# Kernel tuning notes

Hardware: AMD Instinct MI355X
Metric: run time of the kernel (lower is better)

The kernel has to match this reference:

```python
import jax, jax.numpy as jnp
import numpy as np

Q = 8192      # num query tokens
S = 32768     # num support points
E = 131072    # num edges (query<-support neighbor pairs)
D = 256       # token_dim
H = 8         # num_heads
HD = D // H   # head_dim = 32
GEO = 128     # geo mlp_hidden = geo_dim
FFN = 2 * D   # ffn hidden
STAT_IN = 12  # 4 stats * 3 coords
EPS_LN = 1e-5


def gelu(x):
    return jax.nn.gelu(x, approximate=False)  # torch nn.GELU default (erf)


def layernorm(x, g, b):
    m = jnp.mean(x, axis=-1, keepdims=True)
    v = jnp.mean((x - m) ** 2, axis=-1, keepdims=True)
    return (x - m) * jax.lax.rsqrt(v + EPS_LN) * g + b


def setup_inputs() -> dict:
    key = jax.random.key(0)
    ks = jax.random.split(key, 16)
    w = lambda k, shp: jax.random.normal(k, shp, jnp.float32) * 0.02
    return {
        "query_tokens": jax.random.normal(ks[0], (Q, D), jnp.float32),
        "query_pos": jax.random.normal(ks[1], (Q, 3), jnp.float32),
        "support_feats": jax.random.normal(ks[2], (S, D), jnp.float32),
        "support_pos": jax.random.normal(ks[3], (S, 3), jnp.float32),
        "Wq": w(ks[4], (D, D)), "Wk": w(ks[5], (D, D)), "Wv": w(ks[6], (D, D)),
        "Wg": w(ks[7], (GEO, D)),
        "Wo": w(ks[8], (D, D)), "bo": jnp.zeros((D,), jnp.float32),
        "log_tau": jnp.array(0.0, jnp.float32),
        "ln1_g": jnp.ones((D,), jnp.float32), "ln1_b": jnp.zeros((D,), jnp.float32),
        "ln2_g": jnp.ones((D,), jnp.float32), "ln2_b": jnp.zeros((D,), jnp.float32),
        "Wf1": w(ks[9], (D, FFN)), "bf1": jnp.zeros((FFN,), jnp.float32),
        "Wf2": w(ks[10], (FFN, D)), "bf2": jnp.zeros((D,), jnp.float32),
        "Gw1": w(ks[11], (STAT_IN, GEO)), "Gb1": jnp.zeros((GEO,), jnp.float32),
        "Gw2": w(ks[12], (GEO, GEO)), "Gb2": jnp.zeros((GEO,), jnp.float32),
        "q_idx": jnp.sort(jax.random.randint(ks[13], (E,), 0, Q)),
        "s_idx": jax.random.randint(ks[14], (E,), 0, S),
        "num_queries": Q,
    }


def geo_stats(rel, q_idx, num_q):
    # rel: [E,3] relative positions; segmented mean/std/min/max -> [num_q, 12]
    ones = jnp.ones((rel.shape[0], 1), rel.dtype)
    cnt = jnp.maximum(jax.ops.segment_sum(ones, q_idx, num_q), 1.0)  # [Q,1]
    mean = jax.ops.segment_sum(rel, q_idx, num_q) / cnt
    var = jax.ops.segment_sum((rel - mean[q_idx]) ** 2, q_idx, num_q) / cnt
    std = jnp.sqrt(var)
    # torch inits min/max with +/-inf then clamps to [-100,100]; jax segment
    # min/max init with dtype extremes -> same result after clip
    mn = jnp.clip(jax.ops.segment_min(rel, q_idx, num_q), -100.0, 100.0)
    mx = jnp.clip(jax.ops.segment_max(rel, q_idx, num_q), -100.0, 100.0)
    return jnp.concatenate([mean, std, mn, mx], axis=-1)


def reference(query_tokens, query_pos, support_feats, support_pos,
              Wq, Wk, Wv, Wg, Wo, bo, log_tau,
              ln1_g, ln1_b, ln2_g, ln2_b,
              Wf1, bf1, Wf2, bf2, Gw1, Gb1, Gw2, Gb2,
              q_idx, s_idx, num_queries):
    num_q = num_queries
    # ---- statistical geo embedding ----
    rel = support_pos[s_idx] - query_pos[q_idx]                 # [E,3]
    raw = geo_stats(rel, q_idx, num_q)                          # [Q,12]
    geo = gelu(gelu(raw @ Gw1 + Gb1) @ Gw2 + Gb2)               # [Q,GEO]

    # ---- AGNO cross attention (pre-norm) ----
    qt = layernorm(query_tokens, ln1_g, ln1_b)
    Qf = qt @ Wq                                                # [Q,D]
    Kf = support_feats @ Wk                                     # [S,D]
    Vf = support_feats @ Wv                                     # [S,D]
    Gf = geo @ Wg                                               # [Q,D]
    qh = Qf[q_idx].reshape(E, H, HD)
    kh = Kf[s_idx].reshape(E, H, HD)
    vh = Vf[s_idx].reshape(E, H, HD)
    gh = Gf[q_idx].reshape(E, H, HD)
    tau = jnp.exp(log_tau)
    scores = jnp.sum(qh * kh, axis=-1) / (jnp.sqrt(jnp.float32(HD)) * tau)  # [E,H]
    # torch scores_max starts at 0 -> max(0, segment max)
    smax = jnp.maximum(jax.ops.segment_max(scores, q_idx, num_q), 0.0)
    ex = jnp.exp(scores - smax[q_idx])
    ssum = jax.ops.segment_sum(ex, q_idx, num_q)
    alpha = ex / jnp.maximum(ssum[q_idx], 1e-8)                 # [E,H]
    weighted = alpha[..., None] * (vh + gh)                     # [E,H,HD]
    out = jax.ops.segment_sum(weighted, q_idx, num_q)           # [Q,H,HD]
    attn = out.reshape(num_q, D) @ Wo + bo

    # ---- residual + FFN ----
    x = query_tokens + attn
    x = x + gelu(layernorm(x, ln2_g, ln2_b) @ Wf1 + bf1) @ Wf2 + bf2
    return x
```

## Files before the change

### kernel.cpp

```cpp
#include <hip/hip_runtime.h>
#include <math.h>

#define QN 8192
#define SN 32768
#define EN 131072
#define DN 256
#define HN 8
#define HDN 32
#define GEON 128
#define FFNN 512

typedef __attribute__((ext_vector_type(8))) short bf16x8;
typedef __attribute__((ext_vector_type(8))) unsigned short u16x8;
typedef __attribute__((ext_vector_type(4))) unsigned short u16x4;
typedef __attribute__((ext_vector_type(4))) float f32x4;

__device__ __forceinline__ unsigned short f2b(float f) {
  union { float f; unsigned u; } v; v.f = f;
  unsigned u = v.u;
  u += 0x7fffu + ((u >> 16) & 1u);
  return (unsigned short)(u >> 16);
}
__device__ __forceinline__ float b2f(unsigned short h) {
  union { unsigned u; float f; } v; v.u = ((unsigned)h) << 16; return v.f;
}
__device__ __forceinline__ float gelu_f(float x) {
  return 0.5f * x * (1.0f + erff(x * 0.70710678118654752440f));
}

template <int KT>
__device__ __forceinline__ u16x8* lds_gk(unsigned short* base, int row, int col) {
  int g = (col >> 3) ^ (row & 7);
  return reinterpret_cast<u16x8*>(base + row * KT + g * 8);
}

__global__ __launch_bounds__(256) void transpose_weights(
    const float* Wq, const float* Wk, const float* Wv, const float* Wg,
    const float* Wo, const float* Wf1, const float* Wf2,
    unsigned short* WqT, unsigned short* WkvT, unsigned short* WgT,
    unsigned short* WoT, unsigned short* Wf1T, unsigned short* Wf2T) {
  int b = blockIdx.x;
  const float* src; unsigned short* dst; int K, N, tile;
  if (b < 16)       { src = Wq;  dst = WqT;          K = 256; N = 256; tile = b; }
  else if (b < 32)  { src = Wk;  dst = WkvT;         K = 256; N = 256; tile = b - 16; }
  else if (b < 48)  { src = Wv;  dst = WkvT + 65536; K = 256; N = 256; tile = b - 32; }
  else if (b < 56)  { src = Wg;  dst = WgT;          K = 128; N = 256; tile = b - 48; }
  else if (b < 72)  { src = Wo;  dst = WoT;          K = 256; N = 256; tile = b - 56; }
  else if (b < 104) { src = Wf1; dst = Wf1T;         K = 256; N = 512; tile = b - 72; }
  else              { src = Wf2; dst = Wf2T;         K = 512; N = 256; tile = b - 104; }
  int ktiles = K >> 6;
  int k0 = (tile % ktiles) * 64, n0 = (tile / ktiles) * 64;
  __shared__ float ts[64][65];
  int t = threadIdx.x;
  int c4 = (t & 15) * 4;
  int r = t >> 4;
#pragma unroll
  for (int p = 0; p < 4; ++p) {
    int row = p * 16 + r;
    float4 v = *(const float4*)(src + (size_t)(k0 + row) * N + n0 + c4);
    ts[row][c4 + 0] = v.x; ts[row][c4 + 1] = v.y;
    ts[row][c4 + 2] = v.z; ts[row][c4 + 3] = v.w;
  }
  __syncthreads();
#pragma unroll
  for (int p = 0; p < 4; ++p) {
    int n = p * 16 + r;
    ushort4 o;
    o.x = f2b(ts[c4 + 0][n]); o.y = f2b(ts[c4 + 1][n]);
    o.z = f2b(ts[c4 + 2][n]); o.w = f2b(ts[c4 + 3][n]);
    *(ushort4*)(dst + (size_t)(n0 + n) * K + k0 + c4) = o;
  }
}

__global__ __launch_bounds__(256) void seg_offsets(const int* q_idx, int* offs) {
  int i = blockIdx.x * 256 + threadIdx.x;
  if (i > QN) return;
  int lo = 0, hi = EN;
  while (lo < hi) {
    int mid = (lo + hi) >> 1;
    if (q_idx[mid] < i) lo = mid + 1; else hi = mid;
  }
  offs[i] = lo;
}

__global__ __launch_bounds__(256) void geo_stats_kernel(
    const float* qpos, const float* spos, const int* offs, const int* s_idx, float* raw) {
  int q = blockIdx.x * 64 + (threadIdx.x >> 2);
  int sub = threadIdx.x & 3;
  int e0 = offs[q], e1 = offs[q + 1];
  float qx = qpos[q * 3 + 0], qy = qpos[q * 3 + 1], qz = qpos[q * 3 + 2];
  float cnt = 0.f, sx = 0.f, sy = 0.f, sz = 0.f, sxx = 0.f, syy = 0.f, szz = 0.f;
  float mnx = 1e30f, mny = 1e30f, mnz = 1e30f, mxx = -1e30f, mxy = -1e30f, mxz = -1e30f;
  for (int e = e0 + sub; e < e1; e += 4) {
    int s = s_idx[e];
    float rx = spos[s * 3 + 0] - qx;
    float ry = spos[s * 3 + 1] - qy;
    float rz = spos[s * 3 + 2] - qz;
    cnt += 1.f;
    sx += rx; sy += ry; sz += rz;
    sxx += rx * rx; syy += ry * ry; szz += rz * rz;
    mnx = fminf(mnx, rx); mny = fminf(mny, ry); mnz = fminf(mnz, rz);
    mxx = fmaxf(mxx, rx); mxy = fmaxf(mxy, ry); mxz = fmaxf(mxz, rz);
  }
#pragma unroll
  for (int msk = 1; msk <= 2; msk <<= 1) {
    cnt += __shfl_xor(cnt, msk);
    sx += __shfl_xor(sx, msk); sy += __shfl_xor(sy, msk); sz += __shfl_xor(sz, msk);
    sxx += __shfl_xor(sxx, msk); syy += __shfl_xor(syy, msk); szz += __shfl_xor(szz, msk);
    mnx = fminf(mnx, __shfl_xor(mnx, msk));
    mny = fminf(mny, __shfl_xor(mny, msk));
    mnz = fminf(mnz, __shfl_xor(mnz, msk));
    mxx = fmaxf(mxx, __shfl_xor(mxx, msk));
    mxy = fmaxf(mxy, __shfl_xor(mxy, msk));
    mxz = fmaxf(mxz, __shfl_xor(mxz, msk));
  }
  if (sub == 0) {
    float c = fmaxf(cnt, 1.f);
    float mx_ = sx / c, my_ = sy / c, mz_ = sz / c;
    float vx = fmaxf(sxx / c - mx_ * mx_, 0.f);
    float vy = fmaxf(syy / c - my_ * my_, 0.f);
    float vz = fmaxf(szz / c - mz_ * mz_, 0.f);
    float* r = raw + (size_t)q * 12;
    r[0] = mx_; r[1] = my_; r[2] = mz_;
    r[3] = sqrtf(vx); r[4] = sqrtf(vy); r[5] = sqrtf(vz);
    r[6] = fminf(fmaxf(mnx, -100.f), 100.f);
    r[7] = fminf(fmaxf(mny, -100.f), 100.f);
    r[8] = fminf(fmaxf(mnz, -100.f), 100.f);
    r[9] = fminf(fmaxf(mxx, -100.f), 100.f);
    r[10] = fminf(fmaxf(mxy, -100.f), 100.f);
    r[11] = fminf(fmaxf(mxz, -100.f), 100.f);
  }
}

__global__ __launch_bounds__(128) void geo_mlp_kernel(
    const float* raw, const float* Gw1, const float* Gb1,
    const float* Gw2, const float* Gb2, unsigned short* geo_b) {
  int qb = blockIdx.x * 8;
  int j = threadIdx.x;
  __shared__ float rs[8][12];
  __shared__ float h1[8][128];
  if (j < 96) rs[j / 12][j % 12] = raw[(size_t)(qb + j / 12) * 12 + (j % 12)];
  __syncthreads();
  float b1 = Gb1[j];
  float acc[8];
#pragma unroll
  for (int qq = 0; qq < 8; ++qq) acc[qq] = b1;
  for (int i = 0; i < 12; ++i) {
    float w = Gw1[i * GEON + j];
#pragma unroll
    for (int qq = 0; qq < 8; ++qq) acc[qq] += rs[qq][i] * w;
  }
#pragma unroll
  for (int qq = 0; qq < 8; ++qq) h1[qq][j] = gelu_f(acc[qq]);
  __syncthreads();
  float b2 = Gb2[j];
  float acc2[8];
#pragma unroll
  for (int qq = 0; qq < 8; ++qq) acc2[qq] = b2;
  for (int k = 0; k < 128; ++k) {
    float w = Gw2[k * GEON + j];
#pragma unroll
    for (int qq = 0; qq < 8; ++qq) acc2[qq] += h1[qq][k] * w;
  }
#pragma unroll
  for (int qq = 0; qq < 8; ++qq)
    geo_b[(size_t)(qb + qq) * GEON + j] = f2b(gelu_f(acc2[qq]));
}

__global__ __launch_bounds__(256) void ln_kernel(
    const float* x, const float* g, const float* b, unsigned short* out) {
  int row = blockIdx.x * 4 + (threadIdx.x >> 6);
  int lane = threadIdx.x & 63;
  const float* xr = x + (size_t)row * DN;
  float4 v = *(const float4*)(xr + lane * 4);
  float s = v.x + v.y + v.z + v.w;
  float ss = v.x * v.x + v.y * v.y + v.z * v.z + v.w * v.w;
#pragma unroll
  for (int msk = 1; msk <= 32; msk <<= 1) {
    s += __shfl_xor(s, msk);
    ss += __shfl_xor(ss, msk);
  }
  float mean = s * (1.f / 256.f);
  float var = ss * (1.f / 256.f) - mean * mean;
  float rs = 1.0f / sqrtf(var + 1e-5f);
  float4 gg = *(const float4*)(g + lane * 4);
  float4 bb = *(const float4*)(b + lane * 4);
  unsigned short* o = out + (size_t)row * DN + lane * 4;
  o[0] = f2b((v.x - mean) * rs * gg.x + bb.x);
  o[1] = f2b((v.y - mean) * rs * gg.y + bb.y);
  o[2] = f2b((v.z - mean) * rs * gg.z + bb.z);
  o[3] = f2b((v.w - mean) * rs * gg.w + bb.w);
}

__global__ __launch_bounds__(256) void kv_gemm(
    const float* A, const unsigned short* BT, unsigned short* KVb) {
  __shared__ unsigned short As[64 * 256];
  __shared__ unsigned short Bs[32 * 256];
  int t = threadIdx.x;
  int bm = blockIdx.x * 64;
  int w = t >> 6, lane = t & 63;
  int quad = lane >> 4, l16 = lane & 15;
  int wr = w >> 1, wc = w & 1;
  int srow = t >> 2, sub = t & 3;
  {
    const float* Ag = A + (size_t)(bm + srow) * 256 + sub * 64;
#pragma unroll
    for (int i = 0; i < 8; ++i) {
      float4 f0 = *(const float4*)(Ag + i * 8);
      float4 f1 = *(const float4*)(Ag + i * 8 + 4);
      u16x8 u;
      u[0] = f2b(f0.x); u[1] = f2b(f0.y); u[2] = f2b(f0.z); u[3] = f2b(f0.w);
      u[4] = f2b(f1.x); u[5] = f2b(f1.y); u[6] = f2b(f1.z); u[7] = f2b(f1.w);
      *lds_gk<256>(As, srow, sub * 64 + i * 8) = u;
    }
  }
  int brow = t >> 3, bsub = t & 7;
  u16x8 pre[4];
  {
    const unsigned short* Bg = BT + (size_t)brow * 256 + bsub * 32;
#pragma unroll
    for (int i = 0; i < 4; ++i) pre[i] = *reinterpret_cast<const u16x8*>(Bg + i * 8);
  }
  for (int ct = 0; ct < 16; ++ct) {
#pragma unroll
    for (int i = 0; i < 4; ++i)
      *lds_gk<256>(Bs, brow, bsub * 32 + i * 8) = pre[i];
    __syncthreads();
    if (ct < 15) {
      const unsigned short* Bg = BT + (size_t)((ct + 1) * 32 + brow) * 256 + bsub * 32;
#pragma unroll
      for (int i = 0; i < 4; ++i) pre[i] = *reinterpret_cast<const u16x8*>(Bg + i * 8);
    }
    f32x4 acc[2];
    acc[0] = (f32x4){0.f, 0.f, 0.f, 0.f};
    acc[1] = (f32x4){0.f, 0.f, 0.f, 0.f};
#pragma unroll
    for (int k = 0; k < 8; ++k) {
      bf16x8 a0 = *reinterpret_cast<bf16x8*>(lds_gk<256>(As, wr * 32 + l16, k * 32 + quad * 8));
      bf16x8 a1 = *reinterpret_cast<bf16x8*>(lds_gk<256>(As, wr * 32 + 16 + l16, k * 32 + quad * 8));
      bf16x8 b0 = *reinterpret_cast<bf16x8*>(lds_gk<256>(Bs, wc * 16 + l16, k * 32 + quad * 8));
      acc[0] = __builtin_amdgcn_mfma_f32_16x16x32_bf16(a0, b0, acc[0], 0, 0, 0);
      acc[1] = __builtin_amdgcn_mfma_f32_16x16x32_bf16(a1, b0, acc[1], 0, 0, 0);
    }
#pragma unroll
    for (int i = 0; i < 2; ++i)
#pragma unroll
      for (int r = 0; r < 4; ++r) {
        int rw = bm + wr * 32 + i * 16 + quad * 4 + r;
        int col = ct * 32 + wc * 16 + l16;
        KVb[(size_t)rw * 512 + col] = f2b(acc[i][r]);
      }
    __syncthreads();
  }
}

template <bool A_FP32, bool COLGRID, bool HAS_BIAS, bool DO_GELU, bool HAS_RESID, bool STORE_F32>
__global__ __launch_bounds__(256) void gemm64(
    const void* Ap, const unsigned short* BT, int M, int N, int K,
    const float* bias, const float* resid, float* outF, unsigned short* outB) {
  __shared__ unsigned short As[64][40];
  __shared__ unsigned short Bs[64][40];
  int t = threadIdx.x;
  int bm = (COLGRID ? blockIdx.x : blockIdx.y) * 64;
  int bn = (COLGRID ? blockIdx.y : blockIdx.x) * 64;
  int w = t >> 6, lane = t & 63;
  int wr = w >> 1, wc = w & 1;
  int quad = lane >> 4, l16 = lane & 15;
  int row = t >> 2, chunk = t & 3;

  const float* AgF = (const float*)Ap + (size_t)(bm + row) * K + chunk * 8;
  const unsigned short* AgB = (const unsigned short*)Ap + (size_t)(bm + row) * K + chunk * 8;
  const unsigned short* Bg = BT + (size_t)(bn + row) * K + chunk * 8;

  float4 pf0, pf1;
  u16x8 pa, pb;
  if (A_FP32) { pf0 = *(const float4*)AgF; pf1 = *(const float4*)(AgF + 4); }
  else        { pa = *(const u16x8*)AgB; }
  pb = *(const u16x8*)Bg;

  f32x4 acc[2][2];
#pragma unroll
  for (int i = 0; i < 2; ++i)
#pragma unroll
    for (int j = 0; j < 2; ++j) acc[i][j] = (f32x4){0.f, 0.f, 0.f, 0.f};

  for (int k0 = 0; k0 < K; k0 += 32) {
    u16x8 ua;
    if (A_FP32) {
      ua[0] = f2b(pf0.x); ua[1] = f2b(pf0.y); ua[2] = f2b(pf0.z); ua[3] = f2b(pf0.w);
      ua[4] = f2b(pf1.x); ua[5] = f2b(pf1.y); ua[6] = f2b(pf1.z); ua[7] = f2b(pf1.w);
    } else {
      ua = pa;
    }
    *reinterpret_cast<u16x8*>(&As[row][chunk * 8]) = ua;
    *reinterpret_cast<u16x8*>(&Bs[row][chunk * 8]) = pb;
    __syncthreads();
    if (k0 + 32 < K) {
      if (A_FP32) { pf0 = *(const float4*)(AgF + k0 + 32); pf1 = *(const float4*)(AgF + k0 + 36); }
      else        { pa = *(const u16x8*)(AgB + k0 + 32); }
      pb = *(const u16x8*)(Bg + k0 + 32);
    }
    bf16x8 a0 = *reinterpret_cast<const bf16x8*>(&As[wr * 32 + l16][quad * 8]);
    bf16x8 a1 = *reinterpret_cast<const bf16x8*>(&As[wr * 32 + 16 + l16][quad * 8]);
    bf16x8 b0 = *reinterpret_cast<const bf16x8*>(&Bs[wc * 32 + l16][quad * 8]);
    bf16x8 b1 = *reinterpret_cast<const bf16x8*>(&Bs[wc * 32 + 16 + l16][quad * 8]);
    acc[0][0] = __builtin_amdgcn_mfma_f32_16x16x32_bf16(a0, b0, acc[0][0], 0, 0, 0);
    acc[0][1] = __builtin_amdgcn_mfma_f32_16x16x32_bf16(a0, b1, acc[0][1], 0, 0, 0);
    acc[1][0] = __builtin_amdgcn_mfma_f32_16x16x32_bf16(a1, b0, acc[1][0], 0, 0, 0);
    acc[1][1] = __builtin_amdgcn_mfma_f32_16x16x32_bf16(a1, b1, acc[1][1], 0, 0, 0);
    __syncthreads();
  }

#pragma unroll
  for (int i = 0; i < 2; ++i)
#pragma unroll
    for (int j = 0; j < 2; ++j) {
      int col = bn + wc * 32 + j * 16 + l16;
      float bv = HAS_BIAS ? bias[col] : 0.f;
#pragma unroll
      for (int r = 0; r < 4; ++r) {
        int rw = bm + wr * 32 + i * 16 + quad * 4 + r;
        float v = acc[i][j][r] + bv;
        if (DO_GELU) v = gelu_f(v);
        if (HAS_RESID) v += resid[(size_t)rw * N + col];
        if (STORE_F32) outF[(size_t)rw * N + col] = v;
        else outB[(size_t)rw * N + col] = f2b(v);
      }
    }
}

__global__ __launch_bounds__(256) void attn_edge_kernel(
    const unsigned short* Qb, const unsigned short* Gfb, const unsigned short* KVb,
    const int* s_idx, const int* offs, const float* log_tau, unsigned short* attn_b) {
  int q = blockIdx.x * 4 + (threadIdx.x >> 6);
  int lane = threadIdx.x & 63;
  int slot = lane >> 4;
  int sl = lane & 15;
  int d0 = sl * 16;
  int e0 = offs[q], e1 = offs[q + 1];
  float invs = expf(-log_tau[0]) * 0.17677669529663687f;
  u16x8 qu0 = *(const u16x8*)(Qb + (size_t)q * DN + d0);
  u16x8 qu1 = *(const u16x8*)(Qb + (size_t)q * DN + d0 + 8);
  u16x8 gu0 = *(const u16x8*)(Gfb + (size_t)q * DN + d0);
  u16x8 gu1 = *(const u16x8*)(Gfb + (size_t)q * DN + d0 + 8);
  float qf[16], gf[16];
#pragma unroll
  for (int j = 0; j < 8; ++j) {
    qf[j] = b2f(qu0[j]) * invs; qf[j + 8] = b2f(qu1[j]) * invs;
    gf[j] = b2f(gu0[j]);        gf[j + 8] = b2f(gu1[j]);
  }
  const float NEG = -1e30f;
  float m = -INFINITY, l = 0.f;
  float a[16];
#pragma unroll
  for (int j = 0; j < 16; ++j) a[j] = 0.f;
  for (int e = e0; e < e1; e += 4) {
    int ee = e + slot;
    bool valid = ee < e1;
    int s = s_idx[valid ? ee : (e1 - 1)];
    const unsigned short* kr = KVb + (size_t)s * 512 + d0;
    u16x8 ku0 = *(const u16x8*)kr;
    u16x8 ku1 = *(const u16x8*)(kr + 8);
    u16x8 vu0 = *(const u16x8*)(kr + 256);
    u16x8 vu1 = *(const u16x8*)(kr + 264);
    float p = 0.f;
#pragma unroll
    for (int j = 0; j < 8; ++j) {
      p += qf[j] * b2f(ku0[j]);
      p += qf[j + 8] * b2f(ku1[j]);
    }
    p += __shfl_xor(p, 1);
    if (!valid) p = -INFINITY;
    float mnew = fmaxf(m, p);
    float sc = (m > NEG) ? __expf(m - mnew) : 0.f;
    float we = valid ? __expf(p - mnew) : 0.f;
    l = l * sc + we;
#pragma unroll
    for (int j = 0; j < 8; ++j) {
      a[j] = a[j] * sc + we * b2f(vu0[j]);
      a[j + 8] = a[j + 8] * sc + we * b2f(vu1[j]);
    }
    m = mnew;
  }
#pragma unroll
  for (int msk = 16; msk <= 32; msk <<= 1) {
    float om = __shfl_xor(m, msk);
    float ol = __shfl_xor(l, msk);
    float M2 = fmaxf(m, om);
    float ws = (m > NEG) ? __expf(m - M2) : 0.f;
    float wo = (om > NEG) ? __expf(om - M2) : 0.f;
    l = l * ws + ol * wo;
#pragma unroll
    for (int j = 0; j < 16; ++j) {
      float oa = __shfl_xor(a[j], msk);
      a[j] = a[j] * ws + oa * wo;
    }
    m = M2;
  }
  float M = fmaxf(m, 0.f);
  float em = (m > NEG) ? __expf(m - M) : 0.f;
  float denom = fmaxf(l * em, 1e-8f);
  float f = em / denom;
  float sa = l * f;
  if (slot == 0) {
    u16x8 o0, o1;
#pragma unroll
    for (int j = 0; j < 8; ++j) {
      o0[j] = f2b(a[j] * f + gf[j] * sa);
      o1[j] = f2b(a[j + 8] * f + gf[j + 8] * sa);
    }
    *(u16x8*)(attn_b + (size_t)q * DN + d0) = o0;
    *(u16x8*)(attn_b + (size_t)q * DN + d0 + 8) = o1;
  }
}

extern "C" void kernel_launch(void* const* d_in, const int* in_sizes, int n_in,
                              void* d_out, int out_size, void* d_ws, size_t ws_size,
                              hipStream_t stream) {
  const float* query_tokens  = (const float*)d_in[0];
  const float* query_pos     = (const float*)d_in[1];
  const float* support_feats = (const float*)d_in[2];
  const float* support_pos   = (const float*)d_in[3];
  const float* Wq  = (const float*)d_in[4];
  const float* Wk  = (const float*)d_in[5];
  const float* Wv  = (const float*)d_in[6];
  const float* Wg  = (const float*)d_in[7];
  const float* Wo  = (const float*)d_in[8];
  const float* bo  = (const float*)d_in[9];
  const float* log_tau = (const float*)d_in[10];
  const float* ln1_g = (const float*)d_in[11];
  const float* ln1_b = (const float*)d_in[12];
  const float* ln2_g = (const float*)d_in[13];
  const float* ln2_b = (const float*)d_in[14];
  const float* Wf1 = (const float*)d_in[15];
  const float* bf1 = (const float*)d_in[16];
  const float* Wf2 = (const float*)d_in[17];
  const float* bf2 = (const float*)d_in[18];
  const float* Gw1 = (const float*)d_in[19];
  const float* Gb1 = (const float*)d_in[20];
  const float* Gw2 = (const float*)d_in[21];
  const float* Gb2 = (const float*)d_in[22];
  const int* q_idx = (const int*)d_in[23];
  const int* s_idx = (const int*)d_in[24];
  float* out = (float*)d_out;

  char* ws = (char*)d_ws;
  size_t off = 0;
  auto alloc = [&](size_t bytes) -> void* {
    void* p = ws + off;
    off = (off + bytes + 255) & ~(size_t)255;
    return p;
  };
  unsigned short* WqT  = (unsigned short*)alloc(65536 * 2);
  unsigned short* WkvT = (unsigned short*)alloc(131072 * 2);
  unsigned short* WgT  = (unsigned short*)alloc(32768 * 2);
  unsigned short* WoT  = (unsigned short*)alloc(65536 * 2);
  unsigned short* Wf1T = (unsigned short*)alloc(131072 * 2);
  unsigned short* Wf2T = (unsigned short*)alloc(131072 * 2);
  int* offs            = (int*)alloc((QN + 1) * 4);
  float* raw           = (float*)alloc((size_t)QN * 12 * 4);
  unsigned short* geo_b = (unsigned short*)alloc((size_t)QN * GEON * 2);
  unsigned short* qt_b  = (unsigned short*)alloc((size_t)QN * DN * 2);
  unsigned short* Qb    = (unsigned short*)alloc((size_t)QN * DN * 2);
  unsigned short* Gf_b  = (unsigned short*)alloc((size_t)QN * DN * 2);
  unsigned short* KVb   = (unsigned short*)alloc((size_t)SN * 512 * 2);
  unsigned short* attn_b = (unsigned short*)alloc((size_t)QN * DN * 2);
  float* x1             = (float*)alloc((size_t)QN * DN * 4);
  unsigned short* z_b   = (unsigned short*)alloc((size_t)QN * DN * 2);
  unsigned short* h_b   = (unsigned short*)alloc((size_t)QN * FFNN * 2);

  transpose_weights<<<136, 256, 0, stream>>>(Wq, Wk, Wv, Wg, Wo, Wf1, Wf2,
                                             WqT, WkvT, WgT, WoT, Wf1T, Wf2T);
  seg_offsets<<<33, 256, 0, stream>>>(q_idx, offs);
  geo_stats_kernel<<<QN / 64, 256, 0, stream>>>(query_pos, support_pos, offs, s_idx, raw);
  geo_mlp_kernel<<<QN / 8, 128, 0, stream>>>(raw, Gw1, Gb1, Gw2, Gb2, geo_b);
  ln_kernel<<<QN / 4, 256, 0, stream>>>(query_tokens, ln1_g, ln1_b, qt_b);
  kv_gemm<<<SN / 64, 256, 0, stream>>>(support_feats, WkvT, KVb);
  gemm64<false, true, false, false, false, false><<<dim3(QN / 64, DN / 64), 256, 0, stream>>>(
      qt_b, WqT, QN, DN, 256, nullptr, nullptr, nullptr, Qb);
  gemm64<false, true, false, false, false, false><<<dim3(QN / 64, DN / 64), 256, 0, stream>>>(
      geo_b, WgT, QN, DN, 128, nullptr, nullptr, nullptr, Gf_b);
  attn_edge_kernel<<<QN / 4, 256, 0, stream>>>(Qb, Gf_b, KVb, s_idx, offs, log_tau, attn_b);
  gemm64<false, true, true, false, true, true><<<dim3(QN / 64, DN / 64), 256, 0, stream>>>(
      attn_b, WoT, QN, DN, 256, bo, query_tokens, x1, nullptr);
  ln_kernel<<<QN / 4, 256, 0, stream>>>(x1, ln2_g, ln2_b, z_b);
  gemm64<false, true, true, true, false, false><<<dim3(QN / 64, FFNN / 64), 256, 0, stream>>>(
      z_b, Wf1T, QN, FFNN, 256, bf1, nullptr, nullptr, h_b);
  gemm64<false, true, true, false, true, true><<<dim3(QN / 64, DN / 64), 256, 0, stream>>>(
      h_b, Wf2T, QN, DN, 512, bf2, x1, out, nullptr);

  (void)in_sizes; (void)n_in; (void)out_size; (void)ws_size;
}
```

Measured before the change: 247.8 us.

## Merge prep and projection kernels into two heterogeneous fused launches

Folds the weight transpose, segment-offset search and first layernorm into one launch that picks its role from the block index. A second launch does the geo stats, geo MLP and the Wg projection in one block per 64 queries, with the geo features kept in swizzled LDS, and runs the KV and Q GEMMs alongside it. This removes several launches and the raw/geo_b global round trips. The cost is a larger shared-memory footprint (about 52KB) on every block of the second launch, which can lower occupancy for the KV/Q GEMM blocks, and 32-wide register accumulators in the geo MLP.

```diff
diff --git a/kernel.cpp b/kernel.cpp
--- a/kernel.cpp
+++ b/kernel.cpp
@@ -12,7 +12,6 @@
 
 typedef __attribute__((ext_vector_type(8))) short bf16x8;
 typedef __attribute__((ext_vector_type(8))) unsigned short u16x8;
-typedef __attribute__((ext_vector_type(4))) unsigned short u16x4;
 typedef __attribute__((ext_vector_type(4))) float f32x4;
 
 __device__ __forceinline__ unsigned short f2b(float f) {
@@ -33,138 +32,82 @@
   int g = (col >> 3) ^ (row & 7);
   return reinterpret_cast<u16x8*>(base + row * KT + g * 8);
 }
-
-__global__ __launch_bounds__(256) void transpose_weights(
+__device__ __forceinline__ unsigned short* lds_gs128(unsigned short* base, int row, int col) {
+  int g = (col >> 3) ^ (row & 7);
+  return base + row * 128 + g * 8 + (col & 7);
+}
+
+__global__ __launch_bounds__(256) void fused_prep(
     const float* Wq, const float* Wk, const float* Wv, const float* Wg,
     const float* Wo, const float* Wf1, const float* Wf2,
     unsigned short* WqT, unsigned short* WkvT, unsigned short* WgT,
-    unsigned short* WoT, unsigned short* Wf1T, unsigned short* Wf2T) {
+    unsigned short* WoT, unsigned short* Wf1T, unsigned short* Wf2T,
+    const int* q_idx, int* offs,
+    const float* x_ln, const float* lng, const float* lnb, unsigned short* ln_out) {
+  __shared__ float ts[64][65];
   int b = blockIdx.x;
-  const float* src; unsigned short* dst; int K, N, tile;
-  if (b < 16)       { src = Wq;  dst = WqT;          K = 256; N = 256; tile = b; }
-  else if (b < 32)  { src = Wk;  dst = WkvT;         K = 256; N = 256; tile = b - 16; }
-  else if (b < 48)  { src = Wv;  dst = WkvT + 65536; K = 256; N = 256; tile = b - 32; }
-  else if (b < 56)  { src = Wg;  dst = WgT;          K = 128; N = 256; tile = b - 48; }
-  else if (b < 72)  { src = Wo;  dst = WoT;          K = 256; N = 256; tile = b - 56; }
-  else if (b < 104) { src = Wf1; dst = Wf1T;         K = 256; N = 512; tile = b - 72; }
-  else              { src = Wf2; dst = Wf2T;         K = 512; N = 256; tile = b - 104; }
-  int ktiles = K >> 6;
-  int k0 = (tile % ktiles) * 64, n0 = (tile / ktiles) * 64;
-  __shared__ float ts[64][65];
   int t = threadIdx.x;
-  int c4 = (t & 15) * 4;
-  int r = t >> 4;
-#pragma unroll
-  for (int p = 0; p < 4; ++p) {
-    int row = p * 16 + r;
-    float4 v = *(const float4*)(src + (size_t)(k0 + row) * N + n0 + c4);
-    ts[row][c4 + 0] = v.x; ts[row][c4 + 1] = v.y;
-    ts[row][c4 + 2] = v.z; ts[row][c4 + 3] = v.w;
-  }
-  __syncthreads();
-#pragma unroll
-  for (int p = 0; p < 4; ++p) {
-    int n = p * 16 + r;
-    ushort4 o;
-    o.x = f2b(ts[c4 + 0][n]); o.y = f2b(ts[c4 + 1][n]);
-    o.z = f2b(ts[c4 + 2][n]); o.w = f2b(ts[c4 + 3][n]);
-    *(ushort4*)(dst + (size_t)(n0 + n) * K + k0 + c4) = o;
-  }
-}
-
-__global__ __launch_bounds__(256) void seg_offsets(const int* q_idx, int* offs) {
-  int i = blockIdx.x * 256 + threadIdx.x;
-  if (i > QN) return;
-  int lo = 0, hi = EN;
-  while (lo < hi) {
-    int mid = (lo + hi) >> 1;
-    if (q_idx[mid] < i) lo = mid + 1; else hi = mid;
-  }
-  offs[i] = lo;
-}
-
-__global__ __launch_bounds__(256) void geo_stats_kernel(
-    const float* qpos, const float* spos, const int* offs, const int* s_idx, float* raw) {
-  int q = blockIdx.x * 64 + (threadIdx.x >> 2);
-  int sub = threadIdx.x & 3;
-  int e0 = offs[q], e1 = offs[q + 1];
-  float qx = qpos[q * 3 + 0], qy = qpos[q * 3 + 1], qz = qpos[q * 3 + 2];
-  float cnt = 0.f, sx = 0.f, sy = 0.f, sz = 0.f, sxx = 0.f, syy = 0.f, szz = 0.f;
-  float mnx = 1e30f, mny = 1e30f, mnz = 1e30f, mxx = -1e30f, mxy = -1e30f, mxz = -1e30f;
-  for (int e = e0 + sub; e < e1; e += 4) {
-    int s = s_idx[e];
-    float rx = spos[s * 3 + 0] - qx;
-    float ry = spos[s * 3 + 1] - qy;
-    float rz = spos[s * 3 + 2] - qz;
-    cnt += 1.f;
-    sx += rx; sy += ry; sz += rz;
-    sxx += rx * rx; syy += ry * ry; szz += rz * rz;
-    mnx = fminf(mnx, rx); mny = fminf(mny, ry); mnz = fminf(mnz, rz);
-    mxx = fmaxf(mxx, rx); mxy = fmaxf(mxy, ry); mxz = fmaxf(mxz, rz);
-  }
-#pragma unroll
-  for (int msk = 1; msk <= 2; msk <<= 1) {
-    cnt += __shfl_xor(cnt, msk);
-    sx += __shfl_xor(sx, msk); sy += __shfl_xor(sy, msk); sz += __shfl_xor(sz, msk);
-    sxx += __shfl_xor(sxx, msk); syy += __shfl_xor(syy, msk); szz += __shfl_xor(szz, msk);
-    mnx = fminf(mnx, __shfl_xor(mnx, msk));
-    mny = fminf(mny, __shfl_xor(mny, msk));
-    mnz = fminf(mnz, __shfl_xor(mnz, msk));
-    mxx = fmaxf(mxx, __shfl_xor(mxx, msk));
-    mxy = fmaxf(mxy, __shfl_xor(mxy, msk));
-    mxz = fmaxf(mxz, __shfl_xor(mxz, msk));
-  }
-  if (sub == 0) {
-    float c = fmaxf(cnt, 1.f);
-    float mx_ = sx / c, my_ = sy / c, mz_ = sz / c;
-    float vx = fmaxf(sxx / c - mx_ * mx_, 0.f);
-    float vy = fmaxf(syy / c - my_ * my_, 0.f);
-    float vz = fmaxf(szz / c - mz_ * mz_, 0.f);
-    float* r = raw + (size_t)q * 12;
-    r[0] = mx_; r[1] = my_; r[2] = mz_;
-    r[3] = sqrtf(vx); r[4] = sqrtf(vy); r[5] = sqrtf(vz);
-    r[6] = fminf(fmaxf(mnx, -100.f), 100.f);
-    r[7] = fminf(fmaxf(mny, -100.f), 100.f);
-    r[8] = fminf(fmaxf(mnz, -100.f), 100.f);
-    r[9] = fminf(fmaxf(mxx, -100.f), 100.f);
-    r[10] = fminf(fmaxf(mxy, -100.f), 100.f);
-    r[11] = fminf(fmaxf(mxz, -100.f), 100.f);
-  }
-}
-
-__global__ __launch_bounds__(128) void geo_mlp_kernel(
-    const float* raw, const float* Gw1, const float* Gb1,
-    const float* Gw2, const float* Gb2, unsigned short* geo_b) {
-  int qb = blockIdx.x * 8;
-  int j = threadIdx.x;
-  __shared__ float rs[8][12];
-  __shared__ float h1[8][128];
-  if (j < 96) rs[j / 12][j % 12] = raw[(size_t)(qb + j / 12) * 12 + (j % 12)];
-  __syncthreads();
-  float b1 = Gb1[j];
-  float acc[8];
-#pragma unroll
-  for (int qq = 0; qq < 8; ++qq) acc[qq] = b1;
-  for (int i = 0; i < 12; ++i) {
-    float w = Gw1[i * GEON + j];
-#pragma unroll
-    for (int qq = 0; qq < 8; ++qq) acc[qq] += rs[qq][i] * w;
-  }
-#pragma unroll
-  for (int qq = 0; qq < 8; ++qq) h1[qq][j] = gelu_f(acc[qq]);
-  __syncthreads();
-  float b2 = Gb2[j];
-  float acc2[8];
-#pragma unroll
-  for (int qq = 0; qq < 8; ++qq) acc2[qq] = b2;
-  for (int k = 0; k < 128; ++k) {
-    float w = Gw2[k * GEON + j];
-#pragma unroll
-    for (int qq = 0; qq < 8; ++qq) acc2[qq] += h1[qq][k] * w;
-  }
-#pragma unroll
-  for (int qq = 0; qq < 8; ++qq)
-    geo_b[(size_t)(qb + qq) * GEON + j] = f2b(gelu_f(acc2[qq]));
+  if (b < 136) {
+    const float* src; unsigned short* dst; int K, N, tile;
+    if (b < 16)       { src = Wq;  dst = WqT;          K = 256; N = 256; tile = b; }
+    else if (b < 32)  { src = Wk;  dst = WkvT;         K = 256; N = 256; tile = b - 16; }
+    else if (b < 48)  { src = Wv;  dst = WkvT + 65536; K = 256; N = 256; tile = b - 32; }
+    else if (b < 56)  { src = Wg;  dst = WgT;          K = 128; N = 256; tile = b - 48; }
+    else if (b < 72)  { src = Wo;  dst = WoT;          K = 256; N = 256; tile = b - 56; }
+    else if (b < 104) { src = Wf1; dst = Wf1T;         K = 256; N = 512; tile = b - 72; }
+    else              { src = Wf2; dst = Wf2T;         K = 512; N = 256; tile = b - 104; }
+    int ktiles = K >> 6;
+    int k0 = (tile % ktiles) * 64, n0 = (tile / ktiles) * 64;
+    int c4 = (t & 15) * 4;
+    int r = t >> 4;
+#pragma unroll
+    for (int p = 0; p < 4; ++p) {
+      int row = p * 16 + r;
+      float4 v = *(const float4*)(src + (size_t)(k0 + row) * N + n0 + c4);
+      ts[row][c4 + 0] = v.x; ts[row][c4 + 1] = v.y;
+      ts[row][c4 + 2] = v.z; ts[row][c4 + 3] = v.w;
+    }
+    __syncthreads();
+#pragma unroll
+    for (int p = 0; p < 4; ++p) {
+      int n = p * 16 + r;
+      ushort4 o;
+      o.x = f2b(ts[c4 + 0][n]); o.y = f2b(ts[c4 + 1][n]);
+      o.z = f2b(ts[c4 + 2][n]); o.w = f2b(ts[c4 + 3][n]);
+      *(ushort4*)(dst + (size_t)(n0 + n) * K + k0 + c4) = o;
+    }
+  } else if (b < 169) {
+    int i = (b - 136) * 256 + t;
+    if (i > QN) return;
+    int lo = 0, hi = EN;
+    while (lo < hi) {
+      int mid = (lo + hi) >> 1;
+      if (q_idx[mid] < i) lo = mid + 1; else hi = mid;
+    }
+    offs[i] = lo;
+  } else {
+    int row = (b - 169) * 4 + (t >> 6);
+    int lane = t & 63;
+    const float* xr = x_ln + (size_t)row * DN;
+    float4 v = *(const float4*)(xr + lane * 4);
+    float s = v.x + v.y + v.z + v.w;
+    float ss = v.x * v.x + v.y * v.y + v.z * v.z + v.w * v.w;
+#pragma unroll
+    for (int msk = 1; msk <= 32; msk <<= 1) {
+      s += __shfl_xor(s, msk);
+      ss += __shfl_xor(ss, msk);
+    }
+    float mean = s * (1.f / 256.f);
+    float var = ss * (1.f / 256.f) - mean * mean;
+    float rs = 1.0f / sqrtf(var + 1e-5f);
+    float4 gg = *(const float4*)(lng + lane * 4);
+    float4 bb = *(const float4*)(lnb + lane * 4);
+    unsigned short* o = ln_out + (size_t)row * DN + lane * 4;
+    o[0] = f2b((v.x - mean) * rs * gg.x + bb.x);
+    o[1] = f2b((v.y - mean) * rs * gg.y + bb.y);
+    o[2] = f2b((v.z - mean) * rs * gg.z + bb.z);
+    o[3] = f2b((v.w - mean) * rs * gg.w + bb.w);
+  }
 }
 
 __global__ __launch_bounds__(256) void ln_kernel(
@@ -192,12 +135,12 @@
   o[3] = f2b((v.w - mean) * rs * gg.w + bb.w);
 }
 
-__global__ __launch_bounds__(256) void kv_gemm(
-    const float* A, const unsigned short* BT, unsigned short* KVb) {
-  __shared__ unsigned short As[64 * 256];
-  __shared__ unsigned short Bs[32 * 256];
-  int t = threadIdx.x;
-  int bm = blockIdx.x * 64;
+
+__device__ __forceinline__ void kv_body(
+    char* smem, const float* A, const unsigned short* BT, unsigned short* KVb,
+    int bm, int t) {
+  unsigned short* As = (unsigned short*)smem;
+  unsigned short* Bs = (unsigned short*)(smem + 32768);
   int w = t >> 6, lane = t & 63;
   int quad = lane >> 4, l16 = lane & 15;
   int wr = w >> 1, wc = w & 1;
@@ -254,15 +197,13 @@
   }
 }
 
-template <bool A_FP32, bool COLGRID, bool HAS_BIAS, bool DO_GELU, bool HAS_RESID, bool STORE_F32>
-__global__ __launch_bounds__(256) void gemm64(
-    const void* Ap, const unsigned short* BT, int M, int N, int K,
-    const float* bias, const float* resid, float* outF, unsigned short* outB) {
-  __shared__ unsigned short As[64][40];
-  __shared__ unsigned short Bs[64][40];
-  int t = threadIdx.x;
-  int bm = (COLGRID ? blockIdx.x : blockIdx.y) * 64;
-  int bn = (COLGRID ? blockIdx.y : blockIdx.x) * 64;
+template <bool A_FP32, bool HAS_BIAS, bool DO_GELU, bool HAS_RESID, bool STORE_F32>
+__device__ __forceinline__ void gemm64_body(
+    char* smem, const void* Ap, const unsigned short* BT, int N, int K,
+    const float* bias, const float* resid, float* outF, unsigned short* outB,
+    int bm, int bn, int t) {
+  unsigned short (*As)[40] = (unsigned short(*)[40])smem;
+  unsigned short (*Bs)[40] = (unsigned short(*)[40])(smem + 5120);
   int w = t >> 6, lane = t & 63;
   int wr = w >> 1, wc = w & 1;
   int quad = lane >> 4, l16 = lane & 15;
@@ -327,6 +268,173 @@
         else outB[(size_t)rw * N + col] = f2b(v);
       }
     }
+}
+
+__device__ __forceinline__ void geo_body(
+    char* smem, const float* qpos, const float* spos, const int* offs,
+    const int* s_idx, const float* Gw1, const float* Gb1,
+    const float* Gw2, const float* Gb2, const unsigned short* WgT,
+    unsigned short* Gf_b, int qb, int t) {
+  float (*rs)[12] = (float(*)[12])smem;
+  unsigned short* geoL = (unsigned short*)(smem + 3072);
+  float (*h1)[128] = (float(*)[128])(smem + 19456);
+  unsigned short* Bs = (unsigned short*)(smem + 19456);
+
+  {
+    int q = qb + (t >> 2);
+    int sub = t & 3;
+    int e0 = offs[q], e1 = offs[q + 1];
+    float qx = qpos[q * 3 + 0], qy = qpos[q * 3 + 1], qz = qpos[q * 3 + 2];
+    float cnt = 0.f, sx = 0.f, sy = 0.f, sz = 0.f, sxx = 0.f, syy = 0.f, szz = 0.f;
+    float mnx = 1e30f, mny = 1e30f, mnz = 1e30f, mxx = -1e30f, mxy = -1e30f, mxz = -1e30f;
+    for (int e = e0 + sub; e < e1; e += 4) {
+      int s = s_idx[e];
+      float rx = spos[s * 3 + 0] - qx;
+      float ry = spos[s * 3 + 1] - qy;
+      float rz = spos[s * 3 + 2] - qz;
+      cnt += 1.f;
+      sx += rx; sy += ry; sz += rz;
+      sxx += rx * rx; syy += ry * ry; szz += rz * rz;
+      mnx = fminf(mnx, rx); mny = fminf(mny, ry); mnz = fminf(mnz, rz);
+      mxx = fmaxf(mxx, rx); mxy = fmaxf(mxy, ry); mxz = fmaxf(mxz, rz);
+    }
+#pragma unroll
+    for (int msk = 1; msk <= 2; msk <<= 1) {
+      cnt += __shfl_xor(cnt, msk);
+      sx += __shfl_xor(sx, msk); sy += __shfl_xor(sy, msk); sz += __shfl_xor(sz, msk);
+      sxx += __shfl_xor(sxx, msk); syy += __shfl_xor(syy, msk); szz += __shfl_xor(szz, msk);
+      mnx = fminf(mnx, __shfl_xor(mnx, msk));
+      mny = fminf(mny, __shfl_xor(mny, msk));
+      mnz = fminf(mnz, __shfl_xor(mnz, msk));
+      mxx = fmaxf(mxx, __shfl_xor(mxx, msk));
+      mxy = fmaxf(mxy, __shfl_xor(mxy, msk));
+      mxz = fmaxf(mxz, __shfl_xor(mxz, msk));
+    }
+    if (sub == 0) {
+      int qq = t >> 2;
+      float c = fmaxf(cnt, 1.f);
+      float mx_ = sx / c, my_ = sy / c, mz_ = sz / c;
+      float vx = fmaxf(sxx / c - mx_ * mx_, 0.f);
+      float vy = fmaxf(syy / c - my_ * my_, 0.f);
+      float vz = fmaxf(szz / c - mz_ * mz_, 0.f);
+      rs[qq][0] = mx_; rs[qq][1] = my_; rs[qq][2] = mz_;
+      rs[qq][3] = sqrtf(vx); rs[qq][4] = sqrtf(vy); rs[qq][5] = sqrtf(vz);
+      rs[qq][6] = fminf(fmaxf(mnx, -100.f), 100.f);
+      rs[qq][7] = fminf(fmaxf(mny, -100.f), 100.f);
+      rs[qq][8] = fminf(fmaxf(mnz, -100.f), 100.f);
+      rs[qq][9] = fminf(fmaxf(mxx, -100.f), 100.f);
+      rs[qq][10] = fminf(fmaxf(mxy, -100.f), 100.f);
+      rs[qq][11] = fminf(fmaxf(mxz, -100.f), 100.f);
+    }
+  }
+  __syncthreads();
+
+  {
+    int j = t & 127;
+    int grp = t >> 7;
+    int qbase = grp * 32;
+    float acc[32];
+    float b1 = Gb1[j];
+#pragma unroll
+    for (int qq = 0; qq < 32; ++qq) acc[qq] = b1;
+    for (int i = 0; i < 12; ++i) {
+      float wv = Gw1[i * GEON + j];
+#pragma unroll
+      for (int qq = 0; qq < 32; ++qq) acc[qq] += rs[qbase + qq][i] * wv;
+    }
+#pragma unroll
+    for (int qq = 0; qq < 32; ++qq) h1[qbase + qq][j] = gelu_f(acc[qq]);
+    __syncthreads();
+    float b2 = Gb2[j];
+    float acc2[32];
+#pragma unroll
+    for (int qq = 0; qq < 32; ++qq) acc2[qq] = b2;
+    for (int k = 0; k < 128; ++k) {
+      float wv = Gw2[k * GEON + j];
+#pragma unroll
+      for (int qq = 0; qq < 32; ++qq) acc2[qq] += h1[qbase + qq][k] * wv;
+    }
+#pragma unroll
+    for (int qq = 0; qq < 32; ++qq)
+      *lds_gs128(geoL, qbase + qq, j) = f2b(gelu_f(acc2[qq]));
+  }
+  __syncthreads();
+
+  {
+    int w = t >> 6, lane = t & 63;
+    int wr = w >> 1, wc = w & 1;
+    int quad = lane >> 4, l16 = lane & 15;
+    int row = t >> 2, sub = t & 3;
+    for (int ct = 0; ct < 4; ++ct) {
+      int bn = ct * 64;
+      {
+        const unsigned short* Bg = WgT + (size_t)(bn + row) * 128 + sub * 32;
+#pragma unroll
+        for (int i = 0; i < 4; ++i)
+          *lds_gk<128>(Bs, row, sub * 32 + i * 8) = *reinterpret_cast<const u16x8*>(Bg + i * 8);
+      }
+      __syncthreads();
+      f32x4 acc[2][2];
+#pragma unroll
+      for (int i = 0; i < 2; ++i)
+#pragma unroll
+        for (int j = 0; j < 2; ++j) acc[i][j] = (f32x4){0.f, 0.f, 0.f, 0.f};
+#pragma unroll
+      for (int k = 0; k < 4; ++k) {
+        bf16x8 a0 = *reinterpret_cast<bf16x8*>(lds_gk<128>(geoL, wr * 32 + l16, k * 32 + quad * 8));
+        bf16x8 a1 = *reinterpret_cast<bf16x8*>(lds_gk<128>(geoL, wr * 32 + 16 + l16, k * 32 + quad * 8));
+        bf16x8 b0 = *reinterpret_cast<bf16x8*>(lds_gk<128>(Bs, wc * 32 + l16, k * 32 + quad * 8));
+        bf16x8 b1 = *reinterpret_cast<bf16x8*>(lds_gk<128>(Bs, wc * 32 + 16 + l16, k * 32 + quad * 8));
+        acc[0][0] = __builtin_amdgcn_mfma_f32_16x16x32_bf16(a0, b0, acc[0][0], 0, 0, 0);
+        acc[0][1] = __builtin_amdgcn_mfma_f32_16x16x32_bf16(a0, b1, acc[0][1], 0, 0, 0);
+        acc[1][0] = __builtin_amdgcn_mfma_f32_16x16x32_bf16(a1, b0, acc[1][0], 0, 0, 0);
+        acc[1][1] = __builtin_amdgcn_mfma_f32_16x16x32_bf16(a1, b1, acc[1][1], 0, 0, 0);
+      }
+#pragma unroll
+      for (int i = 0; i < 2; ++i)
+#pragma unroll
+        for (int j = 0; j < 2; ++j) {
+          int col = bn + wc * 32 + j * 16 + l16;
+#pragma unroll
+          for (int r = 0; r < 4; ++r) {
+            int rw = qb + wr * 32 + i * 16 + quad * 4 + r;
+            Gf_b[(size_t)rw * 256 + col] = f2b(acc[i][j][r]);
+          }
+        }
+      __syncthreads();
+    }
+  }
+}
+
+__global__ __launch_bounds__(256) void fused_stage2(
+    const float* qpos, const float* spos, const int* offs, const int* s_idx,
+    const float* Gw1, const float* Gb1, const float* Gw2, const float* Gb2,
+    const unsigned short* WgT, unsigned short* Gf_b,
+    const float* support_feats, const unsigned short* WkvT, unsigned short* KVb,
+    const unsigned short* qt_b, const unsigned short* WqT, unsigned short* Qb) {
+  __shared__ __align__(16) char smem[52224];
+  int b = blockIdx.x;
+  int t = threadIdx.x;
+  if (b < 128) {
+    geo_body(smem, qpos, spos, offs, s_idx, Gw1, Gb1, Gw2, Gb2, WgT, Gf_b, b * 64, t);
+  } else if (b < 640) {
+    kv_body(smem, support_feats, WkvT, KVb, (b - 128) * 64, t);
+  } else {
+    int bb = b - 640;
+    int bm = (bb & 127) * 64, bn = (bb >> 7) * 64;
+    gemm64_body<false, false, false, false, false>(
+        smem, qt_b, WqT, DN, 256, nullptr, nullptr, nullptr, Qb, bm, bn, t);
+  }
+}
+
+template <bool A_FP32, bool HAS_BIAS, bool DO_GELU, bool HAS_RESID, bool STORE_F32>
+__global__ __launch_bounds__(256) void gemm64(
+    const void* Ap, const unsigned short* BT, int N, int K,
+    const float* bias, const float* resid, float* outF, unsigned short* outB) {
+  __shared__ __align__(16) char smem[10240];
+  gemm64_body<A_FP32, HAS_BIAS, DO_GELU, HAS_RESID, STORE_F32>(
+      smem, Ap, BT, N, K, bias, resid, outF, outB,
+      blockIdx.x * 64, blockIdx.y * 64, threadIdx.x);
 }
 
 __global__ __launch_bounds__(256) void attn_edge_kernel(
@@ -458,8 +566,6 @@
   unsigned short* Wf1T = (unsigned short*)alloc(131072 * 2);
   unsigned short* Wf2T = (unsigned short*)alloc(131072 * 2);
   int* offs            = (int*)alloc((QN + 1) * 4);
-  float* raw           = (float*)alloc((size_t)QN * 12 * 4);
-  unsigned short* geo_b = (unsigned short*)alloc((size_t)QN * GEON * 2);
   unsigned short* qt_b  = (unsigned short*)alloc((size_t)QN * DN * 2);
   unsigned short* Qb    = (unsigned short*)alloc((size_t)QN * DN * 2);
   unsigned short* Gf_b  = (unsigned short*)alloc((size_t)QN * DN * 2);
@@ -469,25 +575,22 @@
   unsigned short* z_b   = (unsigned short*)alloc((size_t)QN * DN * 2);
   unsigned short* h_b   = (unsigned short*)alloc((size_t)QN * FFNN * 2);
 
-  transpose_weights<<<136, 256, 0, stream>>>(Wq, Wk, Wv, Wg, Wo, Wf1, Wf2,
-                                             WqT, WkvT, WgT, WoT, Wf1T, Wf2T);
-  seg_offsets<<<33, 256, 0, stream>>>(q_idx, offs);
-  geo_stats_kernel<<<QN / 64, 256, 0, stream>>>(query_pos, support_pos, offs, s_idx, raw);
-  geo_mlp_kernel<<<QN / 8, 128, 0, stream>>>(raw, Gw1, Gb1, Gw2, Gb2, geo_b);
-  ln_kernel<<<QN / 4, 256, 0, stream>>>(query_tokens, ln1_g, ln1_b, qt_b);
-  kv_gemm<<<SN / 64, 256, 0, stream>>>(support_feats, WkvT, KVb);
-  gemm64<false, true, false, false, false, false><<<dim3(QN / 64, DN / 64), 256, 0, stream>>>(
-      qt_b, WqT, QN, DN, 256, nullptr, nullptr, nullptr, Qb);
-  gemm64<false, true, false, false, false, false><<<dim3(QN / 64, DN / 64), 256, 0, stream>>>(
-      geo_b, WgT, QN, DN, 128, nullptr, nullptr, nullptr, Gf_b);
+  fused_prep<<<2217, 256, 0, stream>>>(Wq, Wk, Wv, Wg, Wo, Wf1, Wf2,
+                                       WqT, WkvT, WgT, WoT, Wf1T, Wf2T,
+                                       q_idx, offs,
+                                       query_tokens, ln1_g, ln1_b, qt_b);
+  fused_stage2<<<1152, 256, 0, stream>>>(query_pos, support_pos, offs, s_idx,
+                                         Gw1, Gb1, Gw2, Gb2, WgT, Gf_b,
+                                         support_feats, WkvT, KVb,
+                                         qt_b, WqT, Qb);
   attn_edge_kernel<<<QN / 4, 256, 0, stream>>>(Qb, Gf_b, KVb, s_idx, offs, log_tau, attn_b);
-  gemm64<false, true, true, false, true, true><<<dim3(QN / 64, DN / 64), 256, 0, stream>>>(
-      attn_b, WoT, QN, DN, 256, bo, query_tokens, x1, nullptr);
+  gemm64<false, true, false, true, true><<<dim3(QN / 64, DN / 64), 256, 0, stream>>>(
+      attn_b, WoT, DN, 256, bo, query_tokens, x1, nullptr);
   ln_kernel<<<QN / 4, 256, 0, stream>>>(x1, ln2_g, ln2_b, z_b);
-  gemm64<false, true, true, true, false, false><<<dim3(QN / 64, FFNN / 64), 256, 0, stream>>>(
-      z_b, Wf1T, QN, FFNN, 256, bf1, nullptr, nullptr, h_b);
-  gemm64<false, true, true, false, true, true><<<dim3(QN / 64, DN / 64), 256, 0, stream>>>(
-      h_b, Wf2T, QN, DN, 512, bf2, x1, out, nullptr);
+  gemm64<false, true, true, false, false><<<dim3(QN / 64, FFNN / 64), 256, 0, stream>>>(
+      z_b, Wf1T, FFNN, 256, bf1, nullptr, nullptr, h_b);
+  gemm64<false, true, false, true, true><<<dim3(QN / 64, DN / 64), 256, 0, stream>>>(
+      h_b, Wf2T, DN, 512, bf2, x1, out, nullptr);
 
   (void)in_sizes; (void)n_in; (void)out_size; (void)ws_size;
 }
```

Measured after the change: 240.1 us. -3.1%, faster.
